# Kernel optimization log

Hardware: AMD Instinct MI355X
Metric: run time of the kernel (lower is better)

Reference implementation:

```python
import jax, jax.numpy as jnp
import numpy as np

B, E, N = 8, 256, 32          # triples, padded edges per triple, neighbors per edge
D, RD = 512, 768              # graph_dim, relation-semantic dim
R = 2000                      # num relations
L = 2                         # relation-context layers
K = 8                         # top_k neighbor similarity
M, HEADS = 32, 8              # memory tokens, memory-attention heads
HLLM = 4096                   # llm hidden size
EPS = 1e-5


def _ln(x, g, b):
    mu = jnp.mean(x, -1, keepdims=True)
    var = jnp.mean(jnp.square(x - mu), -1, keepdims=True)
    return (x - mu) * jax.lax.rsqrt(var + EPS) * g + b


def setup_inputs() -> dict:
    key = jax.random.key(0)
    ks = iter(jax.random.split(key, 40))
    nrm = lambda shape, s=0.02: jax.random.normal(next(ks), shape, jnp.float32) * s
    return {
        'edge_rel_ids': jax.random.randint(next(ks), (B, E), 0, R, jnp.int32),
        'neighbor_rel_ids': jax.random.randint(next(ks), (B, E, N), 0, R, jnp.int32),
        'edge_mask': jnp.ones((B, E), jnp.float32),
        'rel_emb': nrm((R, RD), 1.0),
        'rp_w': nrm((D, RD)), 'rp_b': jnp.zeros((D,), jnp.float32),
        'ly_vw': nrm((L, D, D)), 'ly_vb': jnp.zeros((L, D), jnp.float32),
        'ly_ow': nrm((L, D, D)), 'ly_ob': jnp.zeros((L, D), jnp.float32),
        'ly_n1g': jnp.ones((L, D), jnp.float32), 'ly_n1b': jnp.zeros((L, D), jnp.float32),
        'ly_n2g': jnp.ones((L, D), jnp.float32), 'ly_n2b': jnp.zeros((L, D), jnp.float32),
        'ly_w1': nrm((L, 4 * D, D)), 'ly_b1': jnp.zeros((L, 4 * D), jnp.float32),
        'ly_w2': nrm((L, D, 4 * D)), 'ly_b2': jnp.zeros((L, D), jnp.float32),
        'mem_q': nrm((M, D)),
        't_qw': nrm((D, D)), 't_qb': jnp.zeros((D,), jnp.float32),
        't_kw': nrm((D, D)), 't_kb': jnp.zeros((D,), jnp.float32),
        't_vw': nrm((D, D)), 't_vb': jnp.zeros((D,), jnp.float32),
        't_ow': nrm((D, D)), 't_ob': jnp.zeros((D,), jnp.float32),
        'proj_w': nrm((HLLM, D)), 'proj_b': jnp.zeros((HLLM,), jnp.float32),
    }


def reference(edge_rel_ids, neighbor_rel_ids, edge_mask, rel_emb, rp_w, rp_b,
              ly_vw, ly_vb, ly_ow, ly_ob, ly_n1g, ly_n1b, ly_n2g, ly_n2b,
              ly_w1, ly_b1, ly_w2, ly_b2, mem_q,
              t_qw, t_qb, t_kw, t_kb, t_vw, t_vb, t_ow, t_ob, proj_w, proj_b):
    rel_vector = lambda ids: rel_emb[ids] @ rp_w.T + rp_b  # embedding gather + rel_proj
    rel_vec = rel_vector(edge_rel_ids)            # [B,E,D]
    neigh = rel_vector(neighbor_rel_ids)          # [B,E,N,D] dominant gather traffic
    # per-edge cosine similarity to neighbor relations, top-k mean aggregation
    rn = rel_vec / jnp.maximum(jnp.linalg.norm(rel_vec, axis=-1, keepdims=True), 1e-12)
    nn_ = neigh / jnp.maximum(jnp.linalg.norm(neigh, axis=-1, keepdims=True), 1e-12)
    sims = jnp.einsum('bend,bed->ben', nn_, rn)   # [B,E,N]
    _, top_idx = jax.lax.top_k(sims, K)           # [B,E,K]
    agg = jnp.take_along_axis(neigh, top_idx[..., None], axis=2).mean(axis=2)  # [B,E,D]
    # RelationContextLayer stack. Each layer attends from one edge-state token to a
    # single context token: softmax over one key is identically 1, so the MHA
    # reduces exactly to out_proj(v_proj(context)) -- same math as torch MHA here.
    states = rel_vec
    for l in range(L):
        attn = (agg @ ly_vw[l].T + ly_vb[l]) @ ly_ow[l].T + ly_ob[l]
        states = _ln(states + attn, ly_n1g[l], ly_n1b[l])
        ff = jax.nn.gelu(states @ ly_w1[l].T + ly_b1[l], approximate=False) @ ly_w2[l].T + ly_b2[l]
        states = _ln(states + ff, ly_n2g[l], ly_n2b[l])
        states = states * edge_mask[..., None]
    # GraphMemoryTokenizer: learned queries cross-attend over padded edge states
    dh = D // HEADS
    q = (mem_q @ t_qw.T + t_qb).reshape(M, HEADS, dh)
    k = (states @ t_kw.T + t_kb).reshape(B, E, HEADS, dh)
    v = (states @ t_vw.T + t_vb).reshape(B, E, HEADS, dh)
    scores = jnp.einsum('mhd,behd->bhme', q, k) / jnp.sqrt(jnp.asarray(dh, q.dtype))
    scores = jnp.where(edge_mask[:, None, None, :] == 0, jnp.finfo(scores.dtype).min, scores)
    attnw = jax.nn.softmax(scores, axis=-1)
    mem = jnp.einsum('bhme,behd->bmhd', attnw, v).reshape(B, M, D)
    mem = mem @ t_ow.T + t_ob
    no_edges = jnp.sum(edge_mask, axis=1) == 0    # rows with zero edges -> zero memory
    mem = jnp.where(no_edges[:, None, None], 0.0, mem)
    return mem @ proj_w.T + proj_b                # [B,M,HLLM]
```

## Files before the change

### kernel.cpp

```cpp
#include <hip/hip_runtime.h>
#include <hip/hip_bf16.h>
#include <math.h>

#define B_   8
#define E_   256
#define N_   32
#define D_   512
#define RD_  768
#define R_   2000
#define L_   2
#define K_   8
#define M_   32
#define H_   8
#define DH_  64
#define HL_  4096

typedef float f32x4 __attribute__((ext_vector_type(4)));
typedef __bf16 bf16x8 __attribute__((ext_vector_type(8)));
typedef const __attribute__((address_space(1))) void GVoid;
typedef __attribute__((address_space(3))) void LVoid;

__device__ __forceinline__ float gelu_exact(float x) {
    return 0.5f * x * (1.0f + erff(x * 0.70710678118654752f));
}
__device__ __forceinline__ unsigned short f2bf(float x) {
    return __hip_bfloat16_raw(__float2bfloat16(x)).x;
}

template <int TM, int TN, int ACT_GELU, int OUT_BF16, int HAS_BIAS>
__global__ __launch_bounds__(256) void gemm_mfma(const unsigned short* __restrict__ A,
                                                 const unsigned short* __restrict__ W,
                                                 const float* __restrict__ bias,
                                                 void* __restrict__ Cv,
                                                 int M, int N, int K) {
    constexpr int WTM = TM / 2, WTN = TN / 2;
    constexpr int RM = WTM / 16, RN = WTN / 16;
    constexpr int AI = TM / 32;
    constexpr int BI = TN / 32;
    __shared__ __align__(16) unsigned short As[TM * 64];
    __shared__ __align__(16) unsigned short Bs[TN * 64];

    const int tid = threadIdx.x;
    const int wave = tid >> 6, lane = tid & 63;
    const int quad = lane >> 4, l16 = lane & 15;
    const int wm = wave >> 1, wn = wave & 1;
    const int bm = blockIdx.y * TM, bn = blockIdx.x * TN;

    const int sub = lane >> 3;
    const int cpr = (lane & 7) ^ sub;

    f32x4 acc[RM][RN];
#pragma unroll
    for (int i = 0; i < RM; i++)
#pragma unroll
        for (int j = 0; j < RN; j++) acc[i][j] = (f32x4){0.f, 0.f, 0.f, 0.f};

    for (int k0 = 0; k0 < K; k0 += 64) {
        __syncthreads();
#pragma unroll
        for (int i = 0; i < AI; i++) {
            int r0 = (wave * AI + i) * 8;
            const unsigned short* g = A + (size_t)(bm + r0 + sub) * K + k0 + cpr * 8;
            __builtin_amdgcn_global_load_lds((GVoid*)g, (LVoid*)&As[r0 * 64], 16, 0, 0);
        }
#pragma unroll
        for (int i = 0; i < BI; i++) {
            int r0 = (wave * BI + i) * 8;
            const unsigned short* g = W + (size_t)(bn + r0 + sub) * K + k0 + cpr * 8;
            __builtin_amdgcn_global_load_lds((GVoid*)g, (LVoid*)&Bs[r0 * 64], 16, 0, 0);
        }
        __syncthreads();

#pragma unroll
        for (int h = 0; h < 2; h++) {
            bf16x8 af[RM], bf[RN];
#pragma unroll
            for (int i = 0; i < RM; i++) {
                int r = wm * WTM + i * 16 + l16;
                int ch = (h * 4 + quad) ^ (r & 7);
                af[i] = *(const bf16x8*)&As[r * 64 + ch * 8];
            }
#pragma unroll
            for (int j = 0; j < RN; j++) {
                int r = wn * WTN + j * 16 + l16;
                int ch = (h * 4 + quad) ^ (r & 7);
                bf[j] = *(const bf16x8*)&Bs[r * 64 + ch * 8];
            }
#pragma unroll
            for (int i = 0; i < RM; i++)
#pragma unroll
                for (int j = 0; j < RN; j++)
                    acc[i][j] = __builtin_amdgcn_mfma_f32_16x16x32_bf16(af[i], bf[j], acc[i][j], 0, 0, 0);
        }
    }

#pragma unroll
    for (int i = 0; i < RM; i++) {
#pragma unroll
        for (int j = 0; j < RN; j++) {
            int c = bn + wn * WTN + j * 16 + l16;
            float bv = HAS_BIAS ? bias[c] : 0.f;
#pragma unroll
            for (int reg = 0; reg < 4; reg++) {
                int r = bm + wm * WTM + i * 16 + quad * 4 + reg;
                if (r < M) {
                    float v = acc[i][j][reg] + bv;
                    if (ACT_GELU) v = gelu_exact(v);
                    if (OUT_BF16)
                        ((unsigned short*)Cv)[(size_t)r * N + c] = f2bf(v);
                    else
                        ((float*)Cv)[(size_t)r * N + c] = v;
                }
            }
        }
    }
}

__global__ void gemm_nt(const float* __restrict__ A, const float* __restrict__ Bm,
                        const float* __restrict__ bias, float* __restrict__ C,
                        int M, int N, int K) {
    __shared__ float As[16][65];
    __shared__ float Bs[16][65];
    const int tid = threadIdx.x;
    const int bm = blockIdx.y * 64, bn = blockIdx.x * 64;
    const int tx = tid & 15, ty = tid >> 4;
    const int lrow = tid >> 2, lk = (tid & 3) << 2;
    float acc[4][4] = {{0.f}};
    const int arow = bm + lrow, brow = bn + lrow;
    for (int k0 = 0; k0 < K; k0 += 16) {
        float4 a4 = make_float4(0.f, 0.f, 0.f, 0.f);
        if (arow < M) a4 = *(const float4*)(A + (size_t)arow * K + k0 + lk);
        float4 b4 = *(const float4*)(Bm + (size_t)brow * K + k0 + lk);
        __syncthreads();
        As[lk + 0][lrow] = a4.x; As[lk + 1][lrow] = a4.y;
        As[lk + 2][lrow] = a4.z; As[lk + 3][lrow] = a4.w;
        Bs[lk + 0][lrow] = b4.x; Bs[lk + 1][lrow] = b4.y;
        Bs[lk + 2][lrow] = b4.z; Bs[lk + 3][lrow] = b4.w;
        __syncthreads();
#pragma unroll
        for (int kk = 0; kk < 16; kk++) {
            float av[4], bv[4];
#pragma unroll
            for (int i = 0; i < 4; i++) av[i] = As[kk][ty * 4 + i];
#pragma unroll
            for (int j = 0; j < 4; j++) bv[j] = Bs[kk][tx * 4 + j];
#pragma unroll
            for (int i = 0; i < 4; i++)
#pragma unroll
                for (int j = 0; j < 4; j++) acc[i][j] += av[i] * bv[j];
        }
    }
#pragma unroll
    for (int i = 0; i < 4; i++) {
        int r = bm + ty * 4 + i;
        if (r >= M) continue;
#pragma unroll
        for (int j = 0; j < 4; j++) {
            int c = bn + tx * 4 + j;
            C[(size_t)r * N + c] = acc[i][j] + bias[c];
        }
    }
}

struct CvtTable {
    const float* src[9];
    unsigned short* dst[9];
    int cum4[10];
};
__global__ void cvt_multi(CvtTable t, int total4) {
    int i = blockIdx.x * 256 + threadIdx.x;
    if (i >= total4) return;
    int k = 0;
#pragma unroll
    for (int j = 0; j < 8; j++) if (i >= t.cum4[j + 1]) k = j + 1;
    int o = i - t.cum4[k];
    float4 v = ((const float4*)t.src[k])[o];
    ushort4 u;
    u.x = f2bf(v.x); u.y = f2bf(v.y); u.z = f2bf(v.z); u.w = f2bf(v.w);
    ((ushort4*)t.dst[k])[o] = u;
}

__global__ void cvt_transpose512(const float* __restrict__ vw, unsigned short* __restrict__ vwT) {
    __shared__ float tile[32][33];
    int l = blockIdx.z;
    int j0 = blockIdx.y * 32, k0 = blockIdx.x * 32;
    const float* src = vw + (size_t)l * 512 * 512;
    for (int r = threadIdx.y; r < 32; r += 8)
        tile[r][threadIdx.x] = src[(size_t)(j0 + r) * 512 + k0 + threadIdx.x];
    __syncthreads();
    unsigned short* dst = vwT + (size_t)l * 512 * 512;
    for (int r = threadIdx.y; r < 32; r += 8)
        dst[(size_t)(k0 + r) * 512 + j0 + threadIdx.x] = f2bf(tile[threadIdx.x][r]);
}

__global__ void prep_small(const float* __restrict__ ow, const float* __restrict__ vb,
                           const float* __restrict__ ob, const float* __restrict__ kb,
                           const float* __restrict__ vb2, float* __restrict__ bfuse,
                           float* __restrict__ kvb) {
    int n = blockIdx.x, z = blockIdx.y, lane = threadIdx.x;
    if (z == 2) {
        if (lane == 0) { kvb[n] = kb[n]; kvb[n + 512] = vb2[n]; }
        return;
    }
    const float* owr = ow + (size_t)z * 512 * 512 + (size_t)n * 512;
    const float* vbr = vb + (size_t)z * 512;
    float s = 0.f;
#pragma unroll
    for (int j = 0; j < 8; j++) s += owr[lane + 64 * j] * vbr[lane + 64 * j];
#pragma unroll
    for (int off = 32; off; off >>= 1) s += __shfl_xor(s, off, 64);
    if (lane == 0) bfuse[z * 512 + n] = s + ob[z * 512 + n];
}

__global__ void rnorm_kernel(const float* __restrict__ proj, float* __restrict__ rn) {
    int r = blockIdx.x, lane = threadIdx.x;
    const float* p = proj + (size_t)r * D_;
    float s = 0.f;
#pragma unroll
    for (int j = 0; j < 8; j++) { float v = p[lane + 64 * j]; s += v * v; }
#pragma unroll
    for (int off = 32; off; off >>= 1) s += __shfl_xor(s, off, 64);
    if (lane == 0) rn[r] = sqrtf(s);
}

__global__ void sim_topk_agg(const int* __restrict__ eids, const int* __restrict__ nids,
                             const float* __restrict__ proj, const float* __restrict__ rn,
                             unsigned short* __restrict__ agg_bf, float* __restrict__ states) {
    int be = blockIdx.x, tid = threadIdx.x;
    __shared__ float ev[512];
    __shared__ float sims[32];
    __shared__ int nid_s[32];
    __shared__ int sel[8];

    int eid = eids[be];
    const float* ep = proj + (size_t)eid * D_;
    float e0 = ep[tid], e1 = ep[tid + 256];
    ev[tid] = e0; ev[tid + 256] = e1;
    states[(size_t)be * D_ + tid] = e0;
    states[(size_t)be * D_ + tid + 256] = e1;
    if (tid < 32) nid_s[tid] = nids[be * N_ + tid];
    __syncthreads();

    int wid = tid >> 6, lane = tid & 63;
    float en = fmaxf(rn[eid], 1e-12f);
    for (int n = wid; n < N_; n += 4) {
        int nid = nid_s[n];
        const float* np = proj + (size_t)nid * D_;
        float s = 0.f;
#pragma unroll
        for (int j = 0; j < 8; j++) s += np[lane + 64 * j] * ev[lane + 64 * j];
#pragma unroll
        for (int off = 32; off; off >>= 1) s += __shfl_xor(s, off, 64);
        if (lane == 0) sims[n] = s / (fmaxf(rn[nid], 1e-12f) * en);
    }
    __syncthreads();

    if (tid == 0) {
        unsigned used = 0;
        for (int k = 0; k < K_; k++) {
            float best = -3.402823466e38f; int bi = 0;
            for (int n = 0; n < N_; n++)
                if (!((used >> n) & 1u) && sims[n] > best) { best = sims[n]; bi = n; }
            used |= 1u << bi;
            sel[k] = nid_s[bi];
        }
    }
    __syncthreads();

    float a0 = 0.f, a1 = 0.f;
#pragma unroll
    for (int k = 0; k < K_; k++) {
        const float* sp = proj + (size_t)sel[k] * D_;
        a0 += sp[tid]; a1 += sp[tid + 256];
    }
    agg_bf[(size_t)be * D_ + tid] = f2bf(a0 * 0.125f);
    agg_bf[(size_t)be * D_ + tid + 256] = f2bf(a1 * 0.125f);
}

__global__ void add_ln_kernel(const float* __restrict__ x, const float* __restrict__ y,
                              int ystride, const float* __restrict__ g,
                              const float* __restrict__ bb, const float* __restrict__ mask,
                              float* __restrict__ out, unsigned short* __restrict__ out_bf) {
    int t = blockIdx.x, tid = threadIdx.x;
    const float* xr = x + (size_t)t * D_;
    const float* yr = y + (size_t)t * ystride;
    float x0 = xr[tid] + yr[tid];
    float x1 = xr[tid + 256] + yr[tid + 256];
    __shared__ float red[8];
    float s = x0 + x1;
#pragma unroll
    for (int off = 32; off; off >>= 1) s += __shfl_xor(s, off, 64);
    int wid = tid >> 6;
    if ((tid & 63) == 0) red[wid] = s;
    __syncthreads();
    float mean = (red[0] + red[1] + red[2] + red[3]) * (1.f / 512.f);
    float d0 = x0 - mean, d1 = x1 - mean;
    float v = d0 * d0 + d1 * d1;
#pragma unroll
    for (int off = 32; off; off >>= 1) v += __shfl_xor(v, off, 64);
    if ((tid & 63) == 0) red[4 + wid] = v;
    __syncthreads();
    float var = (red[4] + red[5] + red[6] + red[7]) * (1.f / 512.f);
    float rs = rsqrtf(var + 1e-5f);
    float mv = mask ? mask[t] : 1.f;
    float o0 = (d0 * rs * g[tid] + bb[tid]) * mv;
    float o1 = (d1 * rs * g[tid + 256] + bb[tid + 256]) * mv;
    out[(size_t)t * D_ + tid] = o0;
    out[(size_t)t * D_ + tid + 256] = o1;
    out_bf[(size_t)t * D_ + tid] = f2bf(o0);
    out_bf[(size_t)t * D_ + tid + 256] = f2bf(o1);
}

__global__ void mem_attn(const float* __restrict__ qb, const float* __restrict__ kv,
                         const float* __restrict__ mask, unsigned short* __restrict__ memb) {
    int idx = blockIdx.x;
    int b = idx & 7;
    int h = (idx >> 3) & 7;
    int m = idx >> 6;
    int tid = threadIdx.x;
    __shared__ float qh[64];
    __shared__ float sc[256];
    __shared__ float red[8];
    __shared__ float oacc[4][64];

    float mk = mask[b * E_ + tid];
    if (tid < 64) qh[tid] = qb[m * D_ + h * DH_ + tid];
    __syncthreads();
    const float* kr = kv + ((size_t)(b * E_ + tid)) * 1024 + h * DH_;
    float s = 0.f;
#pragma unroll
    for (int d = 0; d < DH_; d += 4) {
        float4 k4 = *(const float4*)(kr + d);
        s += k4.x * qh[d] + k4.y * qh[d + 1] + k4.z * qh[d + 2] + k4.w * qh[d + 3];
    }
    s *= 0.125f;
    if (mk == 0.f) s = -3.402823466e38f;
    float mx = s;
#pragma unroll
    for (int off = 32; off; off >>= 1) mx = fmaxf(mx, __shfl_xor(mx, off, 64));
    if ((tid & 63) == 0) red[tid >> 6] = mx;
    __syncthreads();
    mx = fmaxf(fmaxf(red[0], red[1]), fmaxf(red[2], red[3]));
    float p = expf(s - mx);
    float sum = p;
#pragma unroll
    for (int off = 32; off; off >>= 1) sum += __shfl_xor(sum, off, 64);
    if ((tid & 63) == 0) red[4 + (tid >> 6)] = sum;
    __syncthreads();
    sum = red[4] + red[5] + red[6] + red[7];
    sc[tid] = p / sum;
    __syncthreads();
    int d = tid & 63, part = tid >> 6;
    const float* vcol = kv + ((size_t)(b * E_ + part * 64)) * 1024 + 512 + h * DH_ + d;
    float acc = 0.f;
#pragma unroll 8
    for (int e = 0; e < 64; e++) acc += sc[part * 64 + e] * vcol[(size_t)e * 1024];
    oacc[part][d] = acc;
    __syncthreads();
    if (part == 0)
        memb[((size_t)(b * M_ + m)) * D_ + h * DH_ + d] =
            f2bf(oacc[0][d] + oacc[1][d] + oacc[2][d] + oacc[3][d]);
}

__global__ void mask_zero(const float* __restrict__ mask, unsigned short* __restrict__ mem2) {
    int b = blockIdx.x, tid = threadIdx.x;
    float s = mask[b * E_ + tid];
    __shared__ float red[4];
#pragma unroll
    for (int off = 32; off; off >>= 1) s += __shfl_xor(s, off, 64);
    if ((tid & 63) == 0) red[tid >> 6] = s;
    __syncthreads();
    if (red[0] + red[1] + red[2] + red[3] == 0.f) {
        for (int i = tid; i < M_ * D_; i += 256)
            mem2[(size_t)b * M_ * D_ + i] = 0;
    }
}

extern "C" void kernel_launch(void* const* d_in, const int* in_sizes, int n_in,
                              void* d_out, int out_size, void* d_ws, size_t ws_size,
                              hipStream_t stream) {
    const int*   edge_rel_ids     = (const int*)d_in[0];
    const int*   neighbor_rel_ids = (const int*)d_in[1];
    const float* edge_mask        = (const float*)d_in[2];
    const float* rel_emb          = (const float*)d_in[3];
    const float* rp_w             = (const float*)d_in[4];
    const float* rp_b             = (const float*)d_in[5];
    const float* ly_vw            = (const float*)d_in[6];
    const float* ly_vb            = (const float*)d_in[7];
    const float* ly_ow            = (const float*)d_in[8];
    const float* ly_ob            = (const float*)d_in[9];
    const float* ly_n1g           = (const float*)d_in[10];
    const float* ly_n1b           = (const float*)d_in[11];
    const float* ly_n2g           = (const float*)d_in[12];
    const float* ly_n2b           = (const float*)d_in[13];
    const float* ly_w1            = (const float*)d_in[14];
    const float* ly_b1            = (const float*)d_in[15];
    const float* ly_w2            = (const float*)d_in[16];
    const float* ly_b2            = (const float*)d_in[17];
    const float* mem_q            = (const float*)d_in[18];
    const float* t_qw             = (const float*)d_in[19];
    const float* t_qb             = (const float*)d_in[20];
    const float* t_kw             = (const float*)d_in[21];
    const float* t_kb             = (const float*)d_in[22];
    const float* t_vw             = (const float*)d_in[23];
    const float* t_vb             = (const float*)d_in[24];
    const float* t_ow             = (const float*)d_in[25];
    const float* t_ob             = (const float*)d_in[26];
    const float* proj_w           = (const float*)d_in[27];
    const float* proj_b           = (const float*)d_in[28];
    float* out = (float*)d_out;
    (void)ws_size; (void)in_sizes; (void)n_in; (void)out_size;

    char* ws = (char*)d_ws;
    size_t off = 0;
    auto allocf = [&](size_t n) { float* p = (float*)(ws + off); off += ((n * 4 + 255) & ~(size_t)255); return p; };
    auto allocb = [&](size_t n) { unsigned short* p = (unsigned short*)(ws + off); off += ((n * 2 + 255) & ~(size_t)255); return p; };

    const int T = B_ * E_;

    float* proj    = allocf((size_t)R_ * D_);
    float* rn      = allocf(R_);
    float* states  = allocf((size_t)T * D_);
    float* tmpB    = allocf((size_t)T * D_);
    float* attnall = allocf((size_t)T * 2 * D_);
    float* qbuf    = allocf((size_t)M_ * D_);
    float* bfuse   = allocf(2 * D_);
    float* kvb     = allocf(2 * D_);
    float* kvbuf   = attnall;

    unsigned short* rel_bf    = allocb((size_t)2048 * RD_);
    unsigned short* rpw_bf    = allocb((size_t)D_ * RD_);
    unsigned short* agg_bf    = allocb((size_t)T * D_);
    unsigned short* states_bf = allocb((size_t)T * D_);
    unsigned short* ff1_bf    = allocb((size_t)T * 4 * D_);
    unsigned short* vwT_bf    = allocb((size_t)L_ * D_ * D_);
    unsigned short* ow_bf     = allocb((size_t)L_ * D_ * D_);
    unsigned short* wfuse_bf  = allocb((size_t)L_ * D_ * D_);
    unsigned short* w1_bf     = allocb((size_t)L_ * 4 * D_ * D_);
    unsigned short* w2_bf     = allocb((size_t)L_ * 4 * D_ * D_);
    unsigned short* kvw_bf    = allocb((size_t)2 * D_ * D_);
    unsigned short* tow_bf    = allocb((size_t)D_ * D_);
    unsigned short* pw_bf     = allocb((size_t)HL_ * D_);
    unsigned short* memb_bf   = allocb((size_t)B_ * M_ * D_);
    unsigned short* mem2_bf   = allocb((size_t)B_ * M_ * D_);

    CvtTable t;
    int sizes[9] = { R_ * RD_, D_ * RD_, L_ * D_ * D_, L_ * 4 * D_ * D_,
                     L_ * 4 * D_ * D_, D_ * D_, D_ * D_, D_ * D_, HL_ * D_ };
    const float* srcs[9] = { rel_emb, rp_w, ly_ow, ly_w1, ly_w2, t_kw, t_vw, t_ow, proj_w };
    unsigned short* dsts[9] = { rel_bf, rpw_bf, ow_bf, w1_bf, w2_bf,
                                kvw_bf, kvw_bf + (size_t)D_ * D_, tow_bf, pw_bf };
    int cum = 0;
    for (int i = 0; i < 9; i++) {
        t.src[i] = srcs[i]; t.dst[i] = dsts[i];
        t.cum4[i] = cum; cum += sizes[i] / 4;
    }
    t.cum4[9] = cum;
    cvt_multi<<<(cum + 255) / 256, 256, 0, stream>>>(t, cum);
    cvt_transpose512<<<dim3(16, 16, 2), dim3(32, 8), 0, stream>>>(ly_vw, vwT_bf);
    prep_small<<<dim3(512, 3), 64, 0, stream>>>(ly_ow, ly_vb, ly_ob, t_kb, t_vb, bfuse, kvb);

    gemm_mfma<32, 64, 0, 0, 1><<<dim3(D_ / 64, 64), 256, 0, stream>>>(
        rel_bf, rpw_bf, rp_b, proj, R_, D_, RD_);
    rnorm_kernel<<<R_, 64, 0, stream>>>(proj, rn);
    sim_topk_agg<<<T, 256, 0, stream>>>(edge_rel_ids, neighbor_rel_ids, proj, rn,
                                        agg_bf, states);

    for (int l = 0; l < L_; l++)
        gemm_mfma<32, 64, 0, 1, 0><<<dim3(8, 16), 256, 0, stream>>>(
            ow_bf + (size_t)l * D_ * D_, vwT_bf + (size_t)l * D_ * D_, nullptr,
            wfuse_bf + (size_t)l * D_ * D_, D_, D_, D_);
    gemm_mfma<64, 64, 0, 0, 1><<<dim3(2 * D_ / 64, T / 64), 256, 0, stream>>>(
        agg_bf, wfuse_bf, bfuse, attnall, T, 2 * D_, D_);

    for (int l = 0; l < L_; l++) {
        add_ln_kernel<<<T, 256, 0, stream>>>(states, attnall + (size_t)l * D_, 2 * D_,
                                             ly_n1g + l * D_, ly_n1b + l * D_, nullptr,
                                             states, states_bf);
        gemm_mfma<64, 64, 1, 1, 1><<<dim3(4 * D_ / 64, T / 64), 256, 0, stream>>>(
            states_bf, w1_bf + (size_t)l * 4 * D_ * D_, ly_b1 + l * 4 * D_,
            ff1_bf, T, 4 * D_, D_);
        gemm_mfma<32, 64, 0, 0, 1><<<dim3(D_ / 64, T / 32), 256, 0, stream>>>(
            ff1_bf, w2_bf + (size_t)l * 4 * D_ * D_, ly_b2 + l * D_,
            tmpB, T, D_, 4 * D_);
        add_ln_kernel<<<T, 256, 0, stream>>>(states, tmpB, D_,
                                             ly_n2g + l * D_, ly_n2b + l * D_, edge_mask,
                                             states, states_bf);
    }

    gemm_mfma<64, 64, 0, 0, 1><<<dim3(2 * D_ / 64, T / 64), 256, 0, stream>>>(
        states_bf, kvw_bf, kvb, kvbuf, T, 2 * D_, D_);
    gemm_nt<<<dim3(D_ / 64, 1), 256, 0, stream>>>(mem_q, t_qw, t_qb, qbuf, M_, D_, D_);

    mem_attn<<<B_ * M_ * H_, 256, 0, stream>>>(qbuf, kvbuf, edge_mask, memb_bf);

    gemm_mfma<32, 64, 0, 1, 1><<<dim3(D_ / 64, 8), 256, 0, stream>>>(
        memb_bf, tow_bf, t_ob, mem2_bf, B_ * M_, D_, D_);
    mask_zero<<<B_, 256, 0, stream>>>(edge_mask, mem2_bf);

    gemm_mfma<32, 64, 0, 0, 1><<<dim3(HL_ / 64, 8), 256, 0, stream>>>(
        mem2_bf, pw_bf, proj_b, out, B_ * M_, HL_, D_);
}
```

Measured before the change: 361.9 us.

## Merge prep kernels, batch wfuse GEMMs, inline row norms, fold mask into GEMM

```diff
diff --git a/kernel.cpp b/kernel.cpp
--- a/kernel.cpp
+++ b/kernel.cpp
@@ -27,12 +27,14 @@
     return __hip_bfloat16_raw(__float2bfloat16(x)).x;
 }
 
-template <int TM, int TN, int ACT_GELU, int OUT_BF16, int HAS_BIAS>
+template <int TM, int TN, int ACT_GELU, int OUT_BF16, int HAS_BIAS, int FLAGS>
 __global__ __launch_bounds__(256) void gemm_mfma(const unsigned short* __restrict__ A,
                                                  const unsigned short* __restrict__ W,
                                                  const float* __restrict__ bias,
                                                  void* __restrict__ Cv,
-                                                 int M, int N, int K) {
+                                                 int M, int N, int K,
+                                                 size_t sA, size_t sW, size_t sC,
+                                                 const float* __restrict__ rowflag) {
     constexpr int WTM = TM / 2, WTN = TN / 2;
     constexpr int RM = WTM / 16, RN = WTN / 16;
     constexpr int AI = TM / 32;
@@ -40,6 +42,9 @@
     __shared__ __align__(16) unsigned short As[TM * 64];
     __shared__ __align__(16) unsigned short Bs[TN * 64];
 
+    const size_t z = blockIdx.z;
+    A += z * sA; W += z * sW;
+
     const int tid = threadIdx.x;
     const int wave = tid >> 6, lane = tid & 63;
     const int quad = lane >> 4, l16 = lane & 15;
@@ -106,125 +111,110 @@
                 if (r < M) {
                     float v = acc[i][j][reg] + bv;
                     if (ACT_GELU) v = gelu_exact(v);
+                    if (FLAGS) v *= rowflag[r >> 5];
                     if (OUT_BF16)
-                        ((unsigned short*)Cv)[(size_t)r * N + c] = f2bf(v);
+                        ((unsigned short*)(Cv))[z * sC + (size_t)r * N + c] = f2bf(v);
                     else
-                        ((float*)Cv)[(size_t)r * N + c] = v;
+                        ((float*)(Cv))[z * sC + (size_t)r * N + c] = v;
                 }
             }
         }
     }
 }
 
-__global__ void gemm_nt(const float* __restrict__ A, const float* __restrict__ Bm,
-                        const float* __restrict__ bias, float* __restrict__ C,
-                        int M, int N, int K) {
-    __shared__ float As[16][65];
-    __shared__ float Bs[16][65];
-    const int tid = threadIdx.x;
-    const int bm = blockIdx.y * 64, bn = blockIdx.x * 64;
-    const int tx = tid & 15, ty = tid >> 4;
-    const int lrow = tid >> 2, lk = (tid & 3) << 2;
-    float acc[4][4] = {{0.f}};
-    const int arow = bm + lrow, brow = bn + lrow;
-    for (int k0 = 0; k0 < K; k0 += 16) {
-        float4 a4 = make_float4(0.f, 0.f, 0.f, 0.f);
-        if (arow < M) a4 = *(const float4*)(A + (size_t)arow * K + k0 + lk);
-        float4 b4 = *(const float4*)(Bm + (size_t)brow * K + k0 + lk);
-        __syncthreads();
-        As[lk + 0][lrow] = a4.x; As[lk + 1][lrow] = a4.y;
-        As[lk + 2][lrow] = a4.z; As[lk + 3][lrow] = a4.w;
-        Bs[lk + 0][lrow] = b4.x; Bs[lk + 1][lrow] = b4.y;
-        Bs[lk + 2][lrow] = b4.z; Bs[lk + 3][lrow] = b4.w;
-        __syncthreads();
-#pragma unroll
-        for (int kk = 0; kk < 16; kk++) {
-            float av[4], bv[4];
-#pragma unroll
-            for (int i = 0; i < 4; i++) av[i] = As[kk][ty * 4 + i];
-#pragma unroll
-            for (int j = 0; j < 4; j++) bv[j] = Bs[kk][tx * 4 + j];
-#pragma unroll
-            for (int i = 0; i < 4; i++)
-#pragma unroll
-                for (int j = 0; j < 4; j++) acc[i][j] += av[i] * bv[j];
-        }
-    }
-#pragma unroll
-    for (int i = 0; i < 4; i++) {
-        int r = bm + ty * 4 + i;
-        if (r >= M) continue;
-#pragma unroll
-        for (int j = 0; j < 4; j++) {
-            int c = bn + tx * 4 + j;
-            C[(size_t)r * N + c] = acc[i][j] + bias[c];
-        }
-    }
-}
-
-struct CvtTable {
+struct PrepArgs {
     const float* src[9];
     unsigned short* dst[9];
     int cum4[10];
+    int nb_cvt, nb_tr, nb_bf, total4;
+    const float* ly_vw; unsigned short* vwT;
+    const float* ly_ow; const float* ly_vb; const float* ly_ob; float* bfuse;
+    const float* t_kb; const float* t_vb; float* kvb;
+    const float* edge_mask; float* flags;
+    const float* mem_q; const float* t_qw; const float* t_qb; float* qbuf;
 };
-__global__ void cvt_multi(CvtTable t, int total4) {
-    int i = blockIdx.x * 256 + threadIdx.x;
-    if (i >= total4) return;
-    int k = 0;
-#pragma unroll
-    for (int j = 0; j < 8; j++) if (i >= t.cum4[j + 1]) k = j + 1;
-    int o = i - t.cum4[k];
-    float4 v = ((const float4*)t.src[k])[o];
-    ushort4 u;
-    u.x = f2bf(v.x); u.y = f2bf(v.y); u.z = f2bf(v.z); u.w = f2bf(v.w);
-    ((ushort4*)t.dst[k])[o] = u;
-}
-
-__global__ void cvt_transpose512(const float* __restrict__ vw, unsigned short* __restrict__ vwT) {
-    __shared__ float tile[32][33];
-    int l = blockIdx.z;
-    int j0 = blockIdx.y * 32, k0 = blockIdx.x * 32;
-    const float* src = vw + (size_t)l * 512 * 512;
-    for (int r = threadIdx.y; r < 32; r += 8)
-        tile[r][threadIdx.x] = src[(size_t)(j0 + r) * 512 + k0 + threadIdx.x];
-    __syncthreads();
-    unsigned short* dst = vwT + (size_t)l * 512 * 512;
-    for (int r = threadIdx.y; r < 32; r += 8)
-        dst[(size_t)(k0 + r) * 512 + j0 + threadIdx.x] = f2bf(tile[threadIdx.x][r]);
-}
-
-__global__ void prep_small(const float* __restrict__ ow, const float* __restrict__ vb,
-                           const float* __restrict__ ob, const float* __restrict__ kb,
-                           const float* __restrict__ vb2, float* __restrict__ bfuse,
-                           float* __restrict__ kvb) {
-    int n = blockIdx.x, z = blockIdx.y, lane = threadIdx.x;
-    if (z == 2) {
-        if (lane == 0) { kvb[n] = kb[n]; kvb[n + 512] = vb2[n]; }
+
+__global__ __launch_bounds__(256) void prep_all(PrepArgs a) {
+    int bx = blockIdx.x, tid = threadIdx.x;
+    if (bx < a.nb_cvt) {
+        int i = bx * 256 + tid;
+        if (i < a.total4) {
+            int k = 0;
+#pragma unroll
+            for (int j = 0; j < 8; j++) if (i >= a.cum4[j + 1]) k = j + 1;
+            int o = i - a.cum4[k];
+            float4 v = ((const float4*)a.src[k])[o];
+            ushort4 u;
+            u.x = f2bf(v.x); u.y = f2bf(v.y); u.z = f2bf(v.z); u.w = f2bf(v.w);
+            ((ushort4*)a.dst[k])[o] = u;
+        }
         return;
     }
-    const float* owr = ow + (size_t)z * 512 * 512 + (size_t)n * 512;
-    const float* vbr = vb + (size_t)z * 512;
-    float s = 0.f;
-#pragma unroll
-    for (int j = 0; j < 8; j++) s += owr[lane + 64 * j] * vbr[lane + 64 * j];
-#pragma unroll
-    for (int off = 32; off; off >>= 1) s += __shfl_xor(s, off, 64);
-    if (lane == 0) bfuse[z * 512 + n] = s + ob[z * 512 + n];
-}
-
-__global__ void rnorm_kernel(const float* __restrict__ proj, float* __restrict__ rn) {
-    int r = blockIdx.x, lane = threadIdx.x;
-    const float* p = proj + (size_t)r * D_;
-    float s = 0.f;
-#pragma unroll
-    for (int j = 0; j < 8; j++) { float v = p[lane + 64 * j]; s += v * v; }
-#pragma unroll
-    for (int off = 32; off; off >>= 1) s += __shfl_xor(s, off, 64);
-    if (lane == 0) rn[r] = sqrtf(s);
+    bx -= a.nb_cvt;
+    if (bx < a.nb_tr) {
+        __shared__ float tile[32][33];
+        int l = bx >> 8, t16 = bx & 255;
+        int j0 = (t16 >> 4) * 32, k0 = (t16 & 15) * 32;
+        int tx = tid & 31, ty = tid >> 5;
+        const float* src = a.ly_vw + (size_t)l * 512 * 512;
+        for (int r = ty; r < 32; r += 8)
+            tile[r][tx] = src[(size_t)(j0 + r) * 512 + k0 + tx];
+        __syncthreads();
+        unsigned short* dst = a.vwT + (size_t)l * 512 * 512;
+        for (int r = ty; r < 32; r += 8)
+            dst[(size_t)(k0 + r) * 512 + j0 + tx] = f2bf(tile[tx][r]);
+        return;
+    }
+    bx -= a.nb_tr;
+    if (bx < a.nb_bf) {
+        int wid = bx * 4 + (tid >> 6);
+        int z = wid >> 9, n = wid & 511, lane = tid & 63;
+        const float* owr = a.ly_ow + (size_t)z * 512 * 512 + (size_t)n * 512;
+        const float* vbr = a.ly_vb + (size_t)z * 512;
+        float s = 0.f;
+#pragma unroll
+        for (int j = 0; j < 8; j++) s += owr[lane + 64 * j] * vbr[lane + 64 * j];
+#pragma unroll
+        for (int off = 32; off; off >>= 1) s += __shfl_xor(s, off, 64);
+        if (lane == 0) a.bfuse[z * 512 + n] = s + a.ly_ob[z * 512 + n];
+        return;
+    }
+    bx -= a.nb_bf;
+    if (bx < 1) {
+        for (int n = tid; n < 512; n += 256) {
+            a.kvb[n] = a.t_kb[n];
+            a.kvb[n + 512] = a.t_vb[n];
+        }
+        __shared__ float red[4];
+        for (int b = 0; b < B_; b++) {
+            float s = a.edge_mask[b * E_ + tid];
+#pragma unroll
+            for (int off = 32; off; off >>= 1) s += __shfl_xor(s, off, 64);
+            if ((tid & 63) == 0) red[tid >> 6] = s;
+            __syncthreads();
+            if (tid == 0)
+                a.flags[b] = (red[0] + red[1] + red[2] + red[3] == 0.f) ? 0.f : 1.f;
+            __syncthreads();
+        }
+        return;
+    }
+    bx -= 1;
+    {
+        int wid = bx * 4 + (tid >> 6);
+        int m = wid >> 9, n = wid & 511, lane = tid & 63;
+        const float* ar = a.mem_q + (size_t)m * 512;
+        const float* br = a.t_qw + (size_t)n * 512;
+        float s = 0.f;
+#pragma unroll
+        for (int j = 0; j < 8; j++) s += ar[lane + 64 * j] * br[lane + 64 * j];
+#pragma unroll
+        for (int off = 32; off; off >>= 1) s += __shfl_xor(s, off, 64);
+        if (lane == 0) a.qbuf[(size_t)m * 512 + n] = s + a.t_qb[n];
+    }
 }
 
 __global__ void sim_topk_agg(const int* __restrict__ eids, const int* __restrict__ nids,
-                             const float* __restrict__ proj, const float* __restrict__ rn,
+                             const float* __restrict__ proj,
                              unsigned short* __restrict__ agg_bf, float* __restrict__ states) {
     int be = blockIdx.x, tid = threadIdx.x;
     __shared__ float ev[512];
@@ -242,16 +232,29 @@
     __syncthreads();
 
     int wid = tid >> 6, lane = tid & 63;
-    float en = fmaxf(rn[eid], 1e-12f);
+    float se = 0.f;
+#pragma unroll
+    for (int j = 0; j < 8; j++) { float v = ev[lane + 64 * j]; se += v * v; }
+#pragma unroll
+    for (int off = 32; off; off >>= 1) se += __shfl_xor(se, off, 64);
+    float en = fmaxf(sqrtf(se), 1e-12f);
+
     for (int n = wid; n < N_; n += 4) {
         int nid = nid_s[n];
         const float* np = proj + (size_t)nid * D_;
-        float s = 0.f;
-#pragma unroll
-        for (int j = 0; j < 8; j++) s += np[lane + 64 * j] * ev[lane + 64 * j];
-#pragma unroll
-        for (int off = 32; off; off >>= 1) s += __shfl_xor(s, off, 64);
-        if (lane == 0) sims[n] = s / (fmaxf(rn[nid], 1e-12f) * en);
+        float s = 0.f, s2 = 0.f;
+#pragma unroll
+        for (int j = 0; j < 8; j++) {
+            float v = np[lane + 64 * j];
+            s += v * ev[lane + 64 * j];
+            s2 += v * v;
+        }
+#pragma unroll
+        for (int off = 32; off; off >>= 1) {
+            s += __shfl_xor(s, off, 64);
+            s2 += __shfl_xor(s2, off, 64);
+        }
+        if (lane == 0) sims[n] = s / (fmaxf(sqrtf(s2), 1e-12f) * en);
     }
     __syncthreads();
 
@@ -360,20 +363,6 @@
     if (part == 0)
         memb[((size_t)(b * M_ + m)) * D_ + h * DH_ + d] =
             f2bf(oacc[0][d] + oacc[1][d] + oacc[2][d] + oacc[3][d]);
-}
-
-__global__ void mask_zero(const float* __restrict__ mask, unsigned short* __restrict__ mem2) {
-    int b = blockIdx.x, tid = threadIdx.x;
-    float s = mask[b * E_ + tid];
-    __shared__ float red[4];
-#pragma unroll
-    for (int off = 32; off; off >>= 1) s += __shfl_xor(s, off, 64);
-    if ((tid & 63) == 0) red[tid >> 6] = s;
-    __syncthreads();
-    if (red[0] + red[1] + red[2] + red[3] == 0.f) {
-        for (int i = tid; i < M_ * D_; i += 256)
-            mem2[(size_t)b * M_ * D_ + i] = 0;
-    }
 }
 
 extern "C" void kernel_launch(void* const* d_in, const int* in_sizes, int n_in,
@@ -419,13 +408,13 @@
     const int T = B_ * E_;
 
     float* proj    = allocf((size_t)R_ * D_);
-    float* rn      = allocf(R_);
     float* states  = allocf((size_t)T * D_);
     float* tmpB    = allocf((size_t)T * D_);
     float* attnall = allocf((size_t)T * 2 * D_);
     float* qbuf    = allocf((size_t)M_ * D_);
     float* bfuse   = allocf(2 * D_);
     float* kvb     = allocf(2 * D_);
+    float* flags   = allocf(B_);
     float* kvbuf   = attnall;
 
     unsigned short* rel_bf    = allocb((size_t)2048 * RD_);
@@ -444,7 +433,7 @@
     unsigned short* memb_bf   = allocb((size_t)B_ * M_ * D_);
     unsigned short* mem2_bf   = allocb((size_t)B_ * M_ * D_);
 
-    CvtTable t;
+    PrepArgs a;
     int sizes[9] = { R_ * RD_, D_ * RD_, L_ * D_ * D_, L_ * 4 * D_ * D_,
                      L_ * 4 * D_ * D_, D_ * D_, D_ * D_, D_ * D_, HL_ * D_ };
     const float* srcs[9] = { rel_emb, rp_w, ly_ow, ly_w1, ly_w2, t_kw, t_vw, t_ow, proj_w };
@@ -452,52 +441,56 @@
                                 kvw_bf, kvw_bf + (size_t)D_ * D_, tow_bf, pw_bf };
     int cum = 0;
     for (int i = 0; i < 9; i++) {
-        t.src[i] = srcs[i]; t.dst[i] = dsts[i];
-        t.cum4[i] = cum; cum += sizes[i] / 4;
-    }
-    t.cum4[9] = cum;
-    cvt_multi<<<(cum + 255) / 256, 256, 0, stream>>>(t, cum);
-    cvt_transpose512<<<dim3(16, 16, 2), dim3(32, 8), 0, stream>>>(ly_vw, vwT_bf);
-    prep_small<<<dim3(512, 3), 64, 0, stream>>>(ly_ow, ly_vb, ly_ob, t_kb, t_vb, bfuse, kvb);
-
-    gemm_mfma<32, 64, 0, 0, 1><<<dim3(D_ / 64, 64), 256, 0, stream>>>(
-        rel_bf, rpw_bf, rp_b, proj, R_, D_, RD_);
-    rnorm_kernel<<<R_, 64, 0, stream>>>(proj, rn);
-    sim_topk_agg<<<T, 256, 0, stream>>>(edge_rel_ids, neighbor_rel_ids, proj, rn,
+        a.src[i] = srcs[i]; a.dst[i] = dsts[i];
+        a.cum4[i] = cum; cum += sizes[i] / 4;
+    }
+    a.cum4[9] = cum;
+    a.total4 = cum;
+    a.nb_cvt = (cum + 255) / 256;
+    a.nb_tr = 512;
+    a.nb_bf = 256;
+    a.ly_vw = ly_vw; a.vwT = vwT_bf;
+    a.ly_ow = ly_ow; a.ly_vb = ly_vb; a.ly_ob = ly_ob; a.bfuse = bfuse;
+    a.t_kb = t_kb; a.t_vb = t_vb; a.kvb = kvb;
+    a.edge_mask = edge_mask; a.flags = flags;
+    a.mem_q = mem_q; a.t_qw = t_qw; a.t_qb = t_qb; a.qbuf = qbuf;
+    int nblk = a.nb_cvt + a.nb_tr + a.nb_bf + 1 + 4096;
+    prep_all<<<nblk, 256, 0, stream>>>(a);
+
+    gemm_mfma<32, 64, 0, 0, 1, 0><<<dim3(D_ / 64, 64), 256, 0, stream>>>(
+        rel_bf, rpw_bf, rp_b, proj, R_, D_, RD_, 0, 0, 0, nullptr);
+    sim_topk_agg<<<T, 256, 0, stream>>>(edge_rel_ids, neighbor_rel_ids, proj,
                                         agg_bf, states);
 
-    for (int l = 0; l < L_; l++)
-        gemm_mfma<32, 64, 0, 1, 0><<<dim3(8, 16), 256, 0, stream>>>(
-            ow_bf + (size_t)l * D_ * D_, vwT_bf + (size_t)l * D_ * D_, nullptr,
-            wfuse_bf + (size_t)l * D_ * D_, D_, D_, D_);
-    gemm_mfma<64, 64, 0, 0, 1><<<dim3(2 * D_ / 64, T / 64), 256, 0, stream>>>(
-        agg_bf, wfuse_bf, bfuse, attnall, T, 2 * D_, D_);
+    gemm_mfma<32, 64, 0, 1, 0, 0><<<dim3(8, 16, 2), 256, 0, stream>>>(
+        ow_bf, vwT_bf, nullptr, wfuse_bf, D_, D_, D_,
+        (size_t)D_ * D_, (size_t)D_ * D_, (size_t)D_ * D_, nullptr);
+    gemm_mfma<64, 64, 0, 0, 1, 0><<<dim3(2 * D_ / 64, T / 64), 256, 0, stream>>>(
+        agg_bf, wfuse_bf, bfuse, attnall, T, 2 * D_, D_, 0, 0, 0, nullptr);
 
     for (int l = 0; l < L_; l++) {
         add_ln_kernel<<<T, 256, 0, stream>>>(states, attnall + (size_t)l * D_, 2 * D_,
                                              ly_n1g + l * D_, ly_n1b + l * D_, nullptr,
                                              states, states_bf);
-        gemm_mfma<64, 64, 1, 1, 1><<<dim3(4 * D_ / 64, T / 64), 256, 0, stream>>>(
+        gemm_mfma<64, 64, 1, 1, 1, 0><<<dim3(4 * D_ / 64, T / 64), 256, 0, stream>>>(
             states_bf, w1_bf + (size_t)l * 4 * D_ * D_, ly_b1 + l * 4 * D_,
-            ff1_bf, T, 4 * D_, D_);
-        gemm_mfma<32, 64, 0, 0, 1><<<dim3(D_ / 64, T / 32), 256, 0, stream>>>(
+            ff1_bf, T, 4 * D_, D_, 0, 0, 0, nullptr);
+        gemm_mfma<32, 64, 0, 0, 1, 0><<<dim3(D_ / 64, T / 32), 256, 0, stream>>>(
             ff1_bf, w2_bf + (size_t)l * 4 * D_ * D_, ly_b2 + l * D_,
-            tmpB, T, D_, 4 * D_);
+            tmpB, T, D_, 4 * D_, 0, 0, 0, nullptr);
         add_ln_kernel<<<T, 256, 0, stream>>>(states, tmpB, D_,
                                              ly_n2g + l * D_, ly_n2b + l * D_, edge_mask,
                                              states, states_bf);
     }
 
-    gemm_mfma<64, 64, 0, 0, 1><<<dim3(2 * D_ / 64, T / 64), 256, 0, stream>>>(
-        states_bf, kvw_bf, kvb, kvbuf, T, 2 * D_, D_);
-    gemm_nt<<<dim3(D_ / 64, 1), 256, 0, stream>>>(mem_q, t_qw, t_qb, qbuf, M_, D_, D_);
+    gemm_mfma<64, 64, 0, 0, 1, 0><<<dim3(2 * D_ / 64, T / 64), 256, 0, stream>>>(
+        states_bf, kvw_bf, kvb, kvbuf, T, 2 * D_, D_, 0, 0, 0, nullptr);
 
     mem_attn<<<B_ * M_ * H_, 256, 0, stream>>>(qbuf, kvbuf, edge_mask, memb_bf);
 
-    gemm_mfma<32, 64, 0, 1, 1><<<dim3(D_ / 64, 8), 256, 0, stream>>>(
-        memb_bf, tow_bf, t_ob, mem2_bf, B_ * M_, D_, D_);
-    mask_zero<<<B_, 256, 0, stream>>>(edge_mask, mem2_bf);
-
-    gemm_mfma<32, 64, 0, 0, 1><<<dim3(HL_ / 64, 8), 256, 0, stream>>>(
-        mem2_bf, pw_bf, proj_b, out, B_ * M_, HL_, D_);
-}
+    gemm_mfma<32, 64, 0, 1, 1, 1><<<dim3(D_ / 64, 8), 256, 0, stream>>>(
+        memb_bf, tow_bf, t_ob, mem2_bf, B_ * M_, D_, D_, 0, 0, 0, flags);
+
+    gemm_mfma<32, 64, 0, 0, 1, 0><<<dim3(HL_ / 64, 8), 256, 0, stream>>>(
+        mem2_bf, pw_bf, proj_b, out, B_ * M_, HL_, D_, 0, 0, 0, nullptr);
+}
```

After: 322.1 us. 1.12x faster.
